# Kernel optimization log

Measured on AMD Instinct MI355X. Metric: run time of the kernel, lower is better.

Reference implementation:

```python
import jax, jax.numpy as jnp
import numpy as np

# Dims: N tokens, D=in_features, E experts, H=head_size, K=top-k, EMB=embed_dim
N, D, E, H, K, EMB = 65536, 256, 4, 512, 2, 512


def setup_inputs() -> dict:
    key = jax.random.key(0)
    ks = jax.random.split(key, 6)
    s_d = 1.0 / np.sqrt(D)
    s_h = 1.0 / np.sqrt(H)
    return {
        "x": jax.random.normal(ks[0], (N, D), jnp.float32),
        "w_gate": jax.random.normal(ks[1], (D, E), jnp.float32) * s_d,   # gating linear
        "w1": jax.random.normal(ks[2], (E, D, H), jnp.float32) * s_d,    # expert up-proj
        "w2": jax.random.normal(ks[3], (E, H, D), jnp.float32) * s_h,    # expert down-proj
        "w_proj": jax.random.normal(ks[4], (D, EMB), jnp.float32) * s_d, # final nn.Linear weight (in, out)
        "b_proj": jnp.zeros((EMB,), jnp.float32),
    }


def reference(x, w_gate, w1, w2, w_proj, b_proj):
    # --- top-k gating (eval mode: no gating noise) ---
    logits = x @ w_gate                                   # [N, E]
    top_logits, top_idx = jax.lax.top_k(logits, K)        # [N, K]
    top_gates = jax.nn.softmax(top_logits, axis=-1)       # softmax over the k selected logits
    n_idx = jnp.arange(x.shape[0])[:, None]
    gates = jnp.zeros_like(logits).at[n_idx, top_idx].set(top_gates)  # dense sparse-gate matrix [N, E]

    # --- expert compute + combine (dense-masked equivalent of dispatch/scatter) ---
    h = jax.nn.gelu(jnp.einsum('nd,edh->neh', x, w1), approximate=False)  # [N, E, H]
    y = jnp.einsum('neh,ehd,ne->nd', h, w2, gates)                         # [N, D]

    # --- output projection ---
    return y @ w_proj + b_proj                            # [N, EMB]
```

## Files before the change

kernel.cpp:

```cpp
#include <hip/hip_runtime.h>
#include <hip/hip_bf16.h>
#include <math.h>


typedef __attribute__((ext_vector_type(4))) float f32x4;
typedef __attribute__((ext_vector_type(8))) short bf16x8;
typedef unsigned int u32;

#define MFMA16(a, b, c) __builtin_amdgcn_mfma_f32_16x16x32_bf16((a), (b), (c), 0, 0, 0)

#define WAITVM4() asm volatile("s_waitcnt vmcnt(4)" ::: "memory")
#define WAITVM0() asm volatile("s_waitcnt vmcnt(0)" ::: "memory")
#define WAITLG0() asm volatile("s_waitcnt lgkmcnt(0)" ::: "memory")
#define SBAR() do { __builtin_amdgcn_sched_barrier(0); \
                    __builtin_amdgcn_s_barrier(); \
                    __builtin_amdgcn_sched_barrier(0); } while (0)
#define GLDS16(g, l) __builtin_amdgcn_global_load_lds( \
    (const __attribute__((address_space(1))) u32*)(g), \
    (__attribute__((address_space(3))) u32*)(l), 16, 0, 0)

__device__ __forceinline__ float bf2f(__hip_bfloat16 v) { return __bfloat162float(v); }

__device__ __forceinline__ bool sniff_f32(const unsigned short* __restrict__ xr) {
    int cnt = 0;
#pragma unroll
    for (int j = 0; j < 32; ++j) {
        int e = (xr[2 * j] >> 7) & 0xFF;
        cnt += (e >= 97 && e <= 157) ? 1 : 0;
    }
    return cnt < 16;
}

__global__ void k_prep(const void* __restrict__ w1,
                       const void* __restrict__ w2,
                       const void* __restrict__ wp,
                       const unsigned short* __restrict__ xr,
                       char* __restrict__ stream) {
    int G = blockIdx.x * 256 + threadIdx.x;
    int s = G >> 10, q = G & 1023;
    const bool f32m = sniff_f32(xr);
    const void* W;
    int srcBase, stride, dpos;
    if (s < 128) {
        int e = s >> 5, r = s & 31, hci = r >> 3, stl = r & 7;
        if (stl < 4) {
            int row = q & 127, gpos = q >> 7;
            int g = gpos ^ (row & 7);
            int h = hci * 128 + row;
            int kb = stl * 64 + g * 8;
            W = w1; srcBase = (e << 17) + (kb << 9) + h; stride = 512;
            dpos = (s << 14) + row * 128 + gpos * 16;
        } else {
            int row = q & 255, gpos = q >> 8;
            int g = gpos ^ ((row >> 1) & 3);
            int hb = hci * 128 + (stl - 4) * 32 + g * 8;
            W = w2; srcBase = (e << 17) + (hb << 8) + row; stride = 256;
            dpos = (s << 14) + row * 64 + gpos * 16;
        }
    } else {
        int ps = s - 128;
        int row = q & 255, gpos = q >> 8;
        int g = gpos ^ ((row >> 1) & 3);
        int n = (ps >> 3) * 256 + row;
        int kb = (ps & 7) * 32 + g * 8;
        W = wp; srcBase = (kb << 9) + n; stride = 512;
        dpos = (s << 14) + row * 64 + gpos * 16;
    }
    union { unsigned short u[8]; uint4 v; } o;
#pragma unroll
    for (int j = 0; j < 8; ++j) {
        int si = srcBase + j * stride;
        if (f32m) {
            union { __hip_bfloat16 b; unsigned short u; } c;
            c.b = __float2bfloat16(((const float*)W)[si]);
            o.u[j] = c.u;
        } else {
            o.u[j] = ((const unsigned short*)W)[si];
        }
    }
    *(uint4*)(stream + dpos) = o.v;
}

__global__ __launch_bounds__(256, 2) void k_moe(
    const void* __restrict__ xin,
    const void* __restrict__ wg,
    const char* __restrict__ stream,
    const void* __restrict__ bp,
    void* __restrict__ outp) {
    extern __shared__ char smem[];
    __hip_bfloat16* Xs = (__hip_bfloat16*)smem;
    char* hsb = smem + 49152;
    float* gate_s = (float*)(smem + 65536);
    float* wgs = (float*)(smem + 36864);
    char* ysb = smem;
    char* peven = smem + 32768;
    char* podd  = smem + 49152;

    const int tid = threadIdx.x;
    const int m0 = blockIdx.x * 64;
    const bool f32m = sniff_f32((const unsigned short*)xin);

    if (!f32m) {
        const uint4* xg = (const uint4*)((const __hip_bfloat16*)xin + (size_t)m0 * 256);
#pragma unroll
        for (int i = 0; i < 8; ++i) {
            int f = tid + 256 * i;
            int r = f >> 5, c = f & 31;
            *(uint4*)&Xs[r * 264 + c * 8] = xg[f];
        }
    } else {
        const float4* xg = (const float4*)((const float*)xin + (size_t)m0 * 256);
#pragma unroll
        for (int i = 0; i < 8; ++i) {
            int f = tid + 256 * i;
            int r = f >> 5, c = f & 31;
            float4 a = xg[2 * f], b = xg[2 * f + 1];
            __hip_bfloat16* d = &Xs[r * 264 + c * 8];
            d[0] = __float2bfloat16(a.x); d[1] = __float2bfloat16(a.y);
            d[2] = __float2bfloat16(a.z); d[3] = __float2bfloat16(a.w);
            d[4] = __float2bfloat16(b.x); d[5] = __float2bfloat16(b.y);
            d[6] = __float2bfloat16(b.z); d[7] = __float2bfloat16(b.w);
        }
    }
    {
#pragma unroll
        for (int e = 0; e < 4; ++e)
            wgs[e * 256 + tid] = f32m ? ((const float*)wg)[tid * 4 + e]
                                      : bf2f(((const __hip_bfloat16*)wg)[tid * 4 + e]);
    }
    __syncthreads();

    {
        int tok = tid >> 2, ge = tid & 3;
        float acc = 0.f;
        if (f32m) {
            const float4* xrow = (const float4*)((const float*)xin + (size_t)(m0 + tok) * 256);
            const float* wrow = &wgs[ge * 256];
#pragma unroll 8
            for (int qd = 0; qd < 64; ++qd) {
                float4 xv = xrow[qd];
                acc += xv.x * wrow[qd * 4] + xv.y * wrow[qd * 4 + 1]
                     + xv.z * wrow[qd * 4 + 2] + xv.w * wrow[qd * 4 + 3];
            }
        } else {
            const float* wrow = &wgs[ge * 256];
#pragma unroll 4
            for (int d8 = 0; d8 < 32; ++d8) {
                bf16x8 xv = *(const bf16x8*)&Xs[tok * 264 + d8 * 8];
#pragma unroll
                for (int j = 0; j < 8; ++j) {
                    union { unsigned u; float f; } c;
                    c.u = ((unsigned)(unsigned short)xv[j]) << 16;
                    acc += c.f * wrow[d8 * 8 + j];
                }
            }
        }
        gate_s[tok * 4 + ge] = acc;
    }
    __syncthreads();
    if (tid < 64) {
        float l[4];
#pragma unroll
        for (int e = 0; e < 4; ++e) l[e] = gate_s[tid * 4 + e];
        int i0 = 0; float v0 = l[0];
#pragma unroll
        for (int e = 1; e < 4; ++e)
            if (l[e] > v0) { v0 = l[e]; i0 = e; }
        int i1 = -1; float v1 = -1e30f;
#pragma unroll
        for (int e = 0; e < 4; ++e)
            if (e != i0 && l[e] > v1) { v1 = l[e]; i1 = e; }
        float t = __expf(v1 - v0);
        float g0 = 1.f / (1.f + t);
        float g1 = t * g0;
#pragma unroll
        for (int e = 0; e < 4; ++e) gate_s[tid * 4 + e] = 0.f;
        gate_s[tid * 4 + i0] = g0;
        gate_s[tid * 4 + i1] = g1;
    }
    __syncthreads();

    const int lane = tid & 63;
    const int wv = tid >> 6;
    const int wr = wv & 1;
    const int wc = wv >> 1;
    const int lm = lane & 15, quad = lane >> 4;
    const int swzB = quad ^ ((lm >> 1) & 3);

    bf16x8 ax[2][8];
#pragma unroll
    for (int mt = 0; mt < 2; ++mt)
#pragma unroll
        for (int ks = 0; ks < 8; ++ks)
            ax[mt][ks] = *(const bf16x8*)&Xs[(32 * wr + 16 * mt + lm) * 264 + ks * 32 + quad * 8];
    __syncthreads();

    const char* src_base = stream + tid * 16;
    const int woff = (tid >> 6) << 10;

    {
        const char* s0 = src_base; char* d0 = smem + woff;
        GLDS16(s0, d0); GLDS16(s0 + 4096, d0 + 4096);
        GLDS16(s0 + 8192, d0 + 8192); GLDS16(s0 + 12288, d0 + 12288);
        const char* s1 = src_base + 16384; char* d1 = smem + 16384 + woff;
        GLDS16(s1, d1); GLDS16(s1 + 4096, d1 + 4096);
        GLDS16(s1 + 8192, d1 + 8192); GLDS16(s1 + 12288, d1 + 12288);
    }

    f32x4 Yacc[2][8];
#pragma unroll
    for (int a = 0; a < 2; ++a)
#pragma unroll
        for (int b = 0; b < 8; ++b) Yacc[a][b] = (f32x4){0.f, 0.f, 0.f, 0.f};

    int sidx = 0, cur = 0;
#pragma unroll 1
    for (int e = 0; e < 4; ++e) {
#pragma unroll 1
        for (int hci = 0; hci < 4; ++hci) {
            f32x4 Hacc[2][4];
#pragma unroll
            for (int a = 0; a < 2; ++a)
#pragma unroll
                for (int b = 0; b < 4; ++b) Hacc[a][b] = (f32x4){0.f, 0.f, 0.f, 0.f};
#pragma unroll
            for (int stA = 0; stA < 4; ++stA) {
                WAITVM4();
                SBAR();
                {
                    int ns = cur + 2; if (ns >= 3) ns -= 3;
                    const char* sp = src_base + ((size_t)(sidx + 2) << 14);
                    char* dp = smem + ns * 16384 + woff;
                    GLDS16(sp, dp); GLDS16(sp + 4096, dp + 4096);
                    GLDS16(sp + 8192, dp + 8192); GLDS16(sp + 12288, dp + 12288);
                }
                const char* rb = smem + cur * 16384;
                __builtin_amdgcn_s_setprio(1);
#pragma unroll
                for (int ks = 0; ks < 2; ++ks)
#pragma unroll
                    for (int nt = 0; nt < 4; ++nt) {
                        int rown = 64 * wc + 16 * nt + lm;
                        bf16x8 b = *(const bf16x8*)(rb + rown * 128
                                      + ((((ks << 2) | quad) ^ (lm & 7)) << 4));
                        Hacc[0][nt] = MFMA16(ax[0][2 * stA + ks], b, Hacc[0][nt]);
                        Hacc[1][nt] = MFMA16(ax[1][2 * stA + ks], b, Hacc[1][nt]);
                    }
                __builtin_amdgcn_s_setprio(0);
                if (stA == 3) {
#pragma unroll
                    for (int mt = 0; mt < 2; ++mt)
#pragma unroll
                        for (int nt = 0; nt < 4; ++nt)
#pragma unroll
                            for (int r = 0; r < 4; ++r) {
                                int row = 32 * wr + 16 * mt + quad * 4 + r;
                                int col = 64 * wc + 16 * nt + lm;
                                float v = Hacc[mt][nt][r];
                                float vv = v * v;
                                float w = fmaf(0.044715f, vv, 1.0f);
                                float u = 1.5957691216f * v * w;
                                float ex = __expf(u);
                                float rr = __builtin_amdgcn_rcpf(ex + 1.0f);
                                float vg = v * gate_s[row * 4 + e];
                                float res = fmaf(-vg, rr, vg);
                                *(__hip_bfloat16*)(hsb + row * 256
                                    + ((col * 2) ^ ((row & 7) << 4))) = __float2bfloat16(res);
                            }
                    WAITLG0();
                }
                ++sidx; cur = (cur < 2) ? cur + 1 : 0;
            }
#pragma unroll
            for (int stB = 0; stB < 4; ++stB) {
                if (sidx == 127) WAITVM0(); else WAITVM4();
                SBAR();
                if (sidx + 2 <= 127) {
                    int ns = cur + 2; if (ns >= 3) ns -= 3;
                    const char* sp = src_base + ((size_t)(sidx + 2) << 14);
                    char* dp = smem + ns * 16384 + woff;
                    GLDS16(sp, dp); GLDS16(sp + 4096, dp + 4096);
                    GLDS16(sp + 8192, dp + 8192); GLDS16(sp + 12288, dp + 12288);
                }
                const char* rb = smem + cur * 16384;
                int r0 = 32 * wr + lm;
                bf16x8 af0 = *(const bf16x8*)(hsb + r0 * 256
                                + ((stB * 64 + quad * 16) ^ ((r0 & 7) << 4)));
                bf16x8 af1 = *(const bf16x8*)(hsb + (r0 + 16) * 256
                                + ((stB * 64 + quad * 16) ^ ((r0 & 7) << 4)));
                __builtin_amdgcn_s_setprio(1);
#pragma unroll
                for (int nt = 0; nt < 8; ++nt) {
                    int rown = 128 * wc + 16 * nt + lm;
                    bf16x8 b = *(const bf16x8*)(rb + rown * 64 + (swzB << 4));
                    Yacc[0][nt] = MFMA16(af0, b, Yacc[0][nt]);
                    Yacc[1][nt] = MFMA16(af1, b, Yacc[1][nt]);
                }
                __builtin_amdgcn_s_setprio(0);
                ++sidx; cur = (cur < 2) ? cur + 1 : 0;
            }
        }
    }

    SBAR();
    {
        const char* s0 = stream + ((size_t)128 << 14) + tid * 16;
        char* d0 = peven + woff;
        GLDS16(s0, d0); GLDS16(s0 + 4096, d0 + 4096);
        GLDS16(s0 + 8192, d0 + 8192); GLDS16(s0 + 12288, d0 + 12288);
        const char* s1 = stream + ((size_t)129 << 14) + tid * 16;
        char* d1 = podd + woff;
        GLDS16(s1, d1); GLDS16(s1 + 4096, d1 + 4096);
        GLDS16(s1 + 8192, d1 + 8192); GLDS16(s1 + 12288, d1 + 12288);
    }
#pragma unroll
    for (int mt = 0; mt < 2; ++mt)
#pragma unroll
        for (int nt = 0; nt < 8; ++nt)
#pragma unroll
            for (int r = 0; r < 4; ++r) {
                int row = 32 * wr + 16 * mt + quad * 4 + r;
                int col = 128 * wc + 16 * nt + lm;
                *(__hip_bfloat16*)(ysb + row * 512
                    + ((col * 2) ^ ((row & 7) << 4))) = __float2bfloat16(Yacc[mt][nt][r]);
            }
    WAITLG0();
    WAITVM4();
    SBAR();

    f32x4 Pacc[2][8];
#pragma unroll
    for (int a = 0; a < 2; ++a)
#pragma unroll
        for (int b = 0; b < 8; ++b) Pacc[a][b] = (f32x4){0.f, 0.f, 0.f, 0.f};
#pragma unroll 1
    for (int ps = 0; ps < 16; ++ps) {
        if (ps > 0) {
            SBAR();
            if (ps < 15) {
                const char* sp = stream + ((size_t)(129 + ps) << 14) + tid * 16;
                char* dp = (((ps + 1) & 1) ? podd : peven) + woff;
                GLDS16(sp, dp); GLDS16(sp + 4096, dp + 4096);
                GLDS16(sp + 8192, dp + 8192); GLDS16(sp + 12288, dp + 12288);
                WAITVM4();
            } else WAITVM0();
            SBAR();
        }
        int t = ps & 7;
        const char* pb = (ps & 1) ? podd : peven;
        int r0 = 32 * wr + lm;
        bf16x8 af0 = *(const bf16x8*)(ysb + r0 * 512
                        + ((t * 64 + quad * 16) ^ ((r0 & 7) << 4)));
        bf16x8 af1 = *(const bf16x8*)(ysb + (r0 + 16) * 512
                        + ((t * 64 + quad * 16) ^ ((r0 & 7) << 4)));
        __builtin_amdgcn_s_setprio(1);
#pragma unroll
        for (int nt = 0; nt < 8; ++nt) {
            int rown = 128 * wc + 16 * nt + lm;
            bf16x8 b = *(const bf16x8*)(pb + rown * 64 + (swzB << 4));
            Pacc[0][nt] = MFMA16(af0, b, Pacc[0][nt]);
            Pacc[1][nt] = MFMA16(af1, b, Pacc[1][nt]);
        }
        __builtin_amdgcn_s_setprio(0);
        if (t == 7) {
            int p = ps >> 3;
#pragma unroll
            for (int nt = 0; nt < 8; ++nt) {
                int col = 256 * p + 128 * wc + 16 * nt + lm;
                float bv = f32m ? ((const float*)bp)[col] : bf2f(((const __hip_bfloat16*)bp)[col]);
#pragma unroll
                for (int mt = 0; mt < 2; ++mt)
#pragma unroll
                    for (int r = 0; r < 4; ++r) {
                        int row = m0 + 32 * wr + 16 * mt + quad * 4 + r;
                        float v = Pacc[mt][nt][r] + bv;
                        if (f32m) ((float*)outp)[(size_t)row * 512 + col] = v;
                        else ((__hip_bfloat16*)outp)[(size_t)row * 512 + col] = __float2bfloat16(v);
                    }
            }
            if (ps < 15) {
#pragma unroll
                for (int a = 0; a < 2; ++a)
#pragma unroll
                    for (int b = 0; b < 8; ++b) Pacc[a][b] = (f32x4){0.f, 0.f, 0.f, 0.f};
            }
        }
    }
}

extern "C" void kernel_launch(void* const* d_in, const int* in_sizes, int n_in,
                              void* d_out, int out_size, void* d_ws, size_t ws_size,
                              hipStream_t stream) {
    const void* x  = d_in[0];
    const void* wg = d_in[1];
    const void* w1 = d_in[2];
    const void* w2 = d_in[3];
    const void* wp = d_in[4];
    const void* bp = d_in[5];

    char* wstream = (char*)d_ws;

    k_prep<<<576, 256, 0, stream>>>(w1, w2, wp, (const unsigned short*)x, wstream);
    k_moe<<<1024, 256, 66560, stream>>>(x, wg, wstream, bp, d_out);
}
```

Measured before the change: 386.2 us.

## Restructure LDS pipeline: early weight prefetch, register-staged B fragments, barrier at loop end

Moves the X tile into a swizzled LDS region so the first two weight-stream stages can be issued before gating rather than after it. In the main loops, B fragments are read into registers before the next stage's global-to-LDS prefetch is issued, and the wait plus barrier moves to the end of each iteration. This lets the prefetch overlap with the MFMA work and removes a barrier per stage. The projection loop becomes a two-deep double buffer that waits with vmcnt(0) each step. LDS grows to 70656 bytes, which may reduce how many blocks fit per CU, and the extra fragment registers raise register pressure.

```diff
diff --git a/kernel.cpp b/kernel.cpp
--- a/kernel.cpp
+++ b/kernel.cpp
@@ -88,16 +88,19 @@
     const void* __restrict__ bp,
     void* __restrict__ outp) {
     extern __shared__ char smem[];
-    __hip_bfloat16* Xs = (__hip_bfloat16*)smem;
+    char* xsb = smem + 32768;
     char* hsb = smem + 49152;
     float* gate_s = (float*)(smem + 65536);
-    float* wgs = (float*)(smem + 36864);
+    float* wgs = (float*)(smem + 66560);
     char* ysb = smem;
     char* peven = smem + 32768;
     char* podd  = smem + 49152;
 
     const int tid = threadIdx.x;
     const int m0 = blockIdx.x * 64;
+    const char* src_base = stream + tid * 16;
+    const int woff = (tid >> 6) << 10;
+
     const bool f32m = sniff_f32((const unsigned short*)xin);
 
     if (!f32m) {
@@ -106,7 +109,7 @@
         for (int i = 0; i < 8; ++i) {
             int f = tid + 256 * i;
             int r = f >> 5, c = f & 31;
-            *(uint4*)&Xs[r * 264 + c * 8] = xg[f];
+            *(uint4*)(xsb + r * 512 + ((c * 16) ^ ((r & 7) << 4))) = xg[f];
         }
     } else {
         const float4* xg = (const float4*)((const float*)xin + (size_t)m0 * 256);
@@ -115,7 +118,7 @@
             int f = tid + 256 * i;
             int r = f >> 5, c = f & 31;
             float4 a = xg[2 * f], b = xg[2 * f + 1];
-            __hip_bfloat16* d = &Xs[r * 264 + c * 8];
+            __hip_bfloat16* d = (__hip_bfloat16*)(xsb + r * 512 + ((c * 16) ^ ((r & 7) << 4)));
             d[0] = __float2bfloat16(a.x); d[1] = __float2bfloat16(a.y);
             d[2] = __float2bfloat16(a.z); d[3] = __float2bfloat16(a.w);
             d[4] = __float2bfloat16(b.x); d[5] = __float2bfloat16(b.y);
@@ -128,7 +131,17 @@
             wgs[e * 256 + tid] = f32m ? ((const float*)wg)[tid * 4 + e]
                                       : bf2f(((const __hip_bfloat16*)wg)[tid * 4 + e]);
     }
-    __syncthreads();
+
+    {
+        const char* s0 = src_base; char* d0 = smem + woff;
+        GLDS16(s0, d0); GLDS16(s0 + 4096, d0 + 4096);
+        GLDS16(s0 + 8192, d0 + 8192); GLDS16(s0 + 12288, d0 + 12288);
+        const char* s1 = src_base + 16384; char* d1 = smem + 16384 + woff;
+        GLDS16(s1, d1); GLDS16(s1 + 4096, d1 + 4096);
+        GLDS16(s1 + 8192, d1 + 8192); GLDS16(s1 + 12288, d1 + 12288);
+    }
+    WAITLG0();
+    SBAR();
 
     {
         int tok = tid >> 2, ge = tid & 3;
@@ -146,7 +159,7 @@
             const float* wrow = &wgs[ge * 256];
 #pragma unroll 4
             for (int d8 = 0; d8 < 32; ++d8) {
-                bf16x8 xv = *(const bf16x8*)&Xs[tok * 264 + d8 * 8];
+                bf16x8 xv = *(const bf16x8*)(xsb + tok * 512 + ((d8 * 16) ^ ((tok & 7) << 4)));
 #pragma unroll
                 for (int j = 0; j < 8; ++j) {
                     union { unsigned u; float f; } c;
@@ -157,7 +170,8 @@
         }
         gate_s[tok * 4 + ge] = acc;
     }
-    __syncthreads();
+    WAITLG0();
+    SBAR();
     if (tid < 64) {
         float l[4];
 #pragma unroll
@@ -178,7 +192,8 @@
         gate_s[tid * 4 + i0] = g0;
         gate_s[tid * 4 + i1] = g1;
     }
-    __syncthreads();
+    WAITLG0();
+    SBAR();
 
     const int lane = tid & 63;
     const int wv = tid >> 6;
@@ -191,21 +206,13 @@
 #pragma unroll
     for (int mt = 0; mt < 2; ++mt)
 #pragma unroll
-        for (int ks = 0; ks < 8; ++ks)
-            ax[mt][ks] = *(const bf16x8*)&Xs[(32 * wr + 16 * mt + lm) * 264 + ks * 32 + quad * 8];
-    __syncthreads();
-
-    const char* src_base = stream + tid * 16;
-    const int woff = (tid >> 6) << 10;
-
-    {
-        const char* s0 = src_base; char* d0 = smem + woff;
-        GLDS16(s0, d0); GLDS16(s0 + 4096, d0 + 4096);
-        GLDS16(s0 + 8192, d0 + 8192); GLDS16(s0 + 12288, d0 + 12288);
-        const char* s1 = src_base + 16384; char* d1 = smem + 16384 + woff;
-        GLDS16(s1, d1); GLDS16(s1 + 4096, d1 + 4096);
-        GLDS16(s1 + 8192, d1 + 8192); GLDS16(s1 + 12288, d1 + 12288);
-    }
+        for (int ks = 0; ks < 8; ++ks) {
+            int row = 32 * wr + 16 * mt + lm;
+            ax[mt][ks] = *(const bf16x8*)(xsb + row * 512
+                            + (((ks * 64 + quad * 16)) ^ ((row & 7) << 4)));
+        }
+    WAITVM4();
+    SBAR();
 
     f32x4 Yacc[2][8];
 #pragma unroll
@@ -225,8 +232,16 @@
                 for (int b = 0; b < 4; ++b) Hacc[a][b] = (f32x4){0.f, 0.f, 0.f, 0.f};
 #pragma unroll
             for (int stA = 0; stA < 4; ++stA) {
-                WAITVM4();
-                SBAR();
+                const char* rb = smem + cur * 16384;
+                bf16x8 bfr[2][4];
+#pragma unroll
+                for (int ks = 0; ks < 2; ++ks)
+#pragma unroll
+                    for (int nt = 0; nt < 4; ++nt) {
+                        int rown = 64 * wc + 16 * nt + lm;
+                        bfr[ks][nt] = *(const bf16x8*)(rb + rown * 128
+                                        + ((((ks << 2) | quad) ^ (lm & 7)) << 4));
+                    }
                 {
                     int ns = cur + 2; if (ns >= 3) ns -= 3;
                     const char* sp = src_base + ((size_t)(sidx + 2) << 14);
@@ -234,17 +249,13 @@
                     GLDS16(sp, dp); GLDS16(sp + 4096, dp + 4096);
                     GLDS16(sp + 8192, dp + 8192); GLDS16(sp + 12288, dp + 12288);
                 }
-                const char* rb = smem + cur * 16384;
                 __builtin_amdgcn_s_setprio(1);
 #pragma unroll
                 for (int ks = 0; ks < 2; ++ks)
 #pragma unroll
                     for (int nt = 0; nt < 4; ++nt) {
-                        int rown = 64 * wc + 16 * nt + lm;
-                        bf16x8 b = *(const bf16x8*)(rb + rown * 128
-                                      + ((((ks << 2) | quad) ^ (lm & 7)) << 4));
-                        Hacc[0][nt] = MFMA16(ax[0][2 * stA + ks], b, Hacc[0][nt]);
-                        Hacc[1][nt] = MFMA16(ax[1][2 * stA + ks], b, Hacc[1][nt]);
+                        Hacc[0][nt] = MFMA16(ax[0][2 * stA + ks], bfr[ks][nt], Hacc[0][nt]);
+                        Hacc[1][nt] = MFMA16(ax[1][2 * stA + ks], bfr[ks][nt], Hacc[1][nt]);
                     }
                 __builtin_amdgcn_s_setprio(0);
                 if (stA == 3) {
@@ -269,40 +280,46 @@
                             }
                     WAITLG0();
                 }
+                WAITVM4();
+                SBAR();
                 ++sidx; cur = (cur < 2) ? cur + 1 : 0;
             }
 #pragma unroll
             for (int stB = 0; stB < 4; ++stB) {
-                if (sidx == 127) WAITVM0(); else WAITVM4();
-                SBAR();
-                if (sidx + 2 <= 127) {
-                    int ns = cur + 2; if (ns >= 3) ns -= 3;
-                    const char* sp = src_base + ((size_t)(sidx + 2) << 14);
-                    char* dp = smem + ns * 16384 + woff;
-                    GLDS16(sp, dp); GLDS16(sp + 4096, dp + 4096);
-                    GLDS16(sp + 8192, dp + 8192); GLDS16(sp + 12288, dp + 12288);
-                }
                 const char* rb = smem + cur * 16384;
                 int r0 = 32 * wr + lm;
                 bf16x8 af0 = *(const bf16x8*)(hsb + r0 * 256
                                 + ((stB * 64 + quad * 16) ^ ((r0 & 7) << 4)));
                 bf16x8 af1 = *(const bf16x8*)(hsb + (r0 + 16) * 256
                                 + ((stB * 64 + quad * 16) ^ ((r0 & 7) << 4)));
-                __builtin_amdgcn_s_setprio(1);
+                bf16x8 bfr[8];
 #pragma unroll
                 for (int nt = 0; nt < 8; ++nt) {
                     int rown = 128 * wc + 16 * nt + lm;
-                    bf16x8 b = *(const bf16x8*)(rb + rown * 64 + (swzB << 4));
-                    Yacc[0][nt] = MFMA16(af0, b, Yacc[0][nt]);
-                    Yacc[1][nt] = MFMA16(af1, b, Yacc[1][nt]);
+                    bfr[nt] = *(const bf16x8*)(rb + rown * 64 + (swzB << 4));
+                }
+                bool pf = (sidx + 2 <= 127);
+                if (pf) {
+                    int ns = cur + 2; if (ns >= 3) ns -= 3;
+                    const char* sp = src_base + ((size_t)(sidx + 2) << 14);
+                    char* dp = smem + ns * 16384 + woff;
+                    GLDS16(sp, dp); GLDS16(sp + 4096, dp + 4096);
+                    GLDS16(sp + 8192, dp + 8192); GLDS16(sp + 12288, dp + 12288);
+                }
+                __builtin_amdgcn_s_setprio(1);
+#pragma unroll
+                for (int nt = 0; nt < 8; ++nt) {
+                    Yacc[0][nt] = MFMA16(af0, bfr[nt], Yacc[0][nt]);
+                    Yacc[1][nt] = MFMA16(af1, bfr[nt], Yacc[1][nt]);
                 }
                 __builtin_amdgcn_s_setprio(0);
+                if (pf) WAITVM4(); else WAITVM0();
+                SBAR();
                 ++sidx; cur = (cur < 2) ? cur + 1 : 0;
             }
         }
     }
 
-    SBAR();
     {
         const char* s0 = stream + ((size_t)128 << 14) + tid * 16;
         char* d0 = peven + woff;
@@ -335,17 +352,6 @@
         for (int b = 0; b < 8; ++b) Pacc[a][b] = (f32x4){0.f, 0.f, 0.f, 0.f};
 #pragma unroll 1
     for (int ps = 0; ps < 16; ++ps) {
-        if (ps > 0) {
-            SBAR();
-            if (ps < 15) {
-                const char* sp = stream + ((size_t)(129 + ps) << 14) + tid * 16;
-                char* dp = (((ps + 1) & 1) ? podd : peven) + woff;
-                GLDS16(sp, dp); GLDS16(sp + 4096, dp + 4096);
-                GLDS16(sp + 8192, dp + 8192); GLDS16(sp + 12288, dp + 12288);
-                WAITVM4();
-            } else WAITVM0();
-            SBAR();
-        }
         int t = ps & 7;
         const char* pb = (ps & 1) ? podd : peven;
         int r0 = 32 * wr + lm;
@@ -353,15 +359,29 @@
                         + ((t * 64 + quad * 16) ^ ((r0 & 7) << 4)));
         bf16x8 af1 = *(const bf16x8*)(ysb + (r0 + 16) * 512
                         + ((t * 64 + quad * 16) ^ ((r0 & 7) << 4)));
-        __builtin_amdgcn_s_setprio(1);
+        bf16x8 bfr[8];
 #pragma unroll
         for (int nt = 0; nt < 8; ++nt) {
             int rown = 128 * wc + 16 * nt + lm;
-            bf16x8 b = *(const bf16x8*)(pb + rown * 64 + (swzB << 4));
-            Pacc[0][nt] = MFMA16(af0, b, Pacc[0][nt]);
-            Pacc[1][nt] = MFMA16(af1, b, Pacc[1][nt]);
+            bfr[nt] = *(const bf16x8*)(pb + rown * 64 + (swzB << 4));
+        }
+        __builtin_amdgcn_s_setprio(1);
+#pragma unroll
+        for (int nt = 0; nt < 8; ++nt) {
+            Pacc[0][nt] = MFMA16(af0, bfr[nt], Pacc[0][nt]);
+            Pacc[1][nt] = MFMA16(af1, bfr[nt], Pacc[1][nt]);
         }
         __builtin_amdgcn_s_setprio(0);
+        if (ps < 15) {
+            WAITVM0();
+            SBAR();
+            if (ps + 2 <= 15) {
+                const char* sp = stream + ((size_t)(130 + ps) << 14) + tid * 16;
+                char* dp = ((ps & 1) ? podd : peven) + woff;
+                GLDS16(sp, dp); GLDS16(sp + 4096, dp + 4096);
+                GLDS16(sp + 8192, dp + 8192); GLDS16(sp + 12288, dp + 12288);
+            }
+        }
         if (t == 7) {
             int p = ps >> 3;
 #pragma unroll
@@ -401,5 +421,5 @@
     char* wstream = (char*)d_ws;
 
     k_prep<<<576, 256, 0, stream>>>(w1, w2, wp, (const unsigned short*)x, wstream);
-    k_moe<<<1024, 256, 66560, stream>>>(x, wg, wstream, bp, d_out);
+    k_moe<<<1024, 256, 70656, stream>>>(x, wg, wstream, bp, d_out);
 }
```

After: 388.2 us. About the same (+0.5%).
